# Performance work log

Hardware: AMD Instinct MI355X
Metric: run time of the kernel (lower is better)

The kernel has to match this reference:

```python
import jax, jax.numpy as jnp
import numpy as np

D_MODEL = 1024
HIDDEN = 1024
N_EXPERTS = 8
TOP_K = 2
BATCH, SEQ = 2, 2048
N_TOKENS = BATCH * SEQ


def setup_inputs() -> dict:
    key = jax.random.key(0)
    ks = jax.random.split(key, 6)
    x = jax.random.normal(ks[0], (BATCH, SEQ, D_MODEL), dtype=jnp.float32)
    expert_weights = jax.random.uniform(ks[1], (N_TOKENS, TOP_K), dtype=jnp.float32)
    expert_indices = jax.random.randint(ks[2], (N_TOKENS, TOP_K), 0, N_EXPERTS, dtype=jnp.int32)
    s_in = 1.0 / np.sqrt(D_MODEL)
    s_hid = 1.0 / np.sqrt(HIDDEN)
    w1 = jax.random.normal(ks[3], (N_EXPERTS, D_MODEL, HIDDEN), dtype=jnp.float32) * s_in
    w3 = jax.random.normal(ks[4], (N_EXPERTS, D_MODEL, HIDDEN), dtype=jnp.float32) * s_in
    w2 = jax.random.normal(ks[5], (N_EXPERTS, HIDDEN, D_MODEL), dtype=jnp.float32) * s_hid
    return {"x": x, "expert_weights": expert_weights, "expert_indices": expert_indices,
            "w1": w1, "w3": w3, "w2": w2}


def reference(x, expert_weights, expert_indices, w1, w3, w2):
    """Dropless MoE MLP (forward_once path): for each token t,
    out[t] = sum_k expert_weights[t,k] * SwiGLU_{expert_indices[t,k]}(x[t]).
    Also returns batch_size_per_expert (histogram of routed assignments).
    """
    d = x.shape[-1]
    xf = x.reshape(-1, d)                                  # [N, d]
    E = w1.shape[0]
    # combine[t, e] = sum over top-k slots routed to expert e of their weight
    onehot = jax.nn.one_hot(expert_indices, E, dtype=xf.dtype)       # [N, K, E]
    combine = jnp.einsum("nk,nke->ne", expert_weights, onehot)      # [N, E]
    out = jnp.zeros_like(xf)
    for e in range(E):  # fixed small loop over experts
        h = jax.nn.silu(xf @ w1[e]) * (xf @ w3[e])          # [N, H]
        out = out + combine[:, e:e + 1] * (h @ w2[e])       # [N, d]
    batch_size_per_expert = jnp.zeros((E,), dtype=jnp.int32).at[
        expert_indices.reshape(-1)].add(1)
    return out.reshape(x.shape), batch_size_per_expert
```

## Files before the change

### kernel.cpp

```cpp
#include <hip/hip_runtime.h>
#include <cstdint>

#define D 1024
#define N_TOKENS 4096
#define N_SLOTS 8192
#define NEXP 8
#define NKT 16
#define MAXT 80

typedef float f32x4 __attribute__((ext_vector_type(4)));
typedef __bf16 bf16x8 __attribute__((ext_vector_type(8)));
typedef __attribute__((address_space(3))) uint32_t lds_u32;
typedef __attribute__((address_space(1))) const uint32_t glb_u32;

__device__ __forceinline__ void gload_lds16(const void* g, void* l) {
  __builtin_amdgcn_global_load_lds((glb_u32*)g, (lds_u32*)l, 16, 0, 0);
}

__device__ __forceinline__ ushort f2bf(float f) {
  union { float f; uint32_t u; } c; c.f = f;
  uint32_t u = c.u;
  return (ushort)((u + 0x7FFFu + ((u >> 16) & 1u)) >> 16);
}

__device__ __forceinline__ float bf2f(ushort u) {
  union { uint32_t u; float f; } c; c.u = (uint32_t)u << 16;
  return c.f;
}

__device__ __forceinline__ bf16x8 lds_frag(const ushort* base, int row, int s) {
  return *(const bf16x8*)((const char*)base + row * 128 + ((s ^ (row & 7)) * 16));
}

#define TPAD 66

__global__ void prep_k(const float* __restrict__ x, const int* __restrict__ ei,
                       const float* __restrict__ ew,
                       const float* __restrict__ w1, const float* __restrict__ w3,
                       float* __restrict__ hist_out, int* __restrict__ meta,
                       int* __restrict__ tok, int* __restrict__ smap,
                       ushort* __restrict__ Xbf, ushort* __restrict__ w13t) {
  int bid = blockIdx.x, t = threadIdx.x;
  if (bid == 0) {
    __shared__ int cmat[256][8];
    __shared__ int off[NEXP + 1];
#pragma unroll
    for (int e = 0; e < NEXP; e++) cmat[t][e] = 0;
    int base = t * 32;
#pragma unroll 4
    for (int j = 0; j < 32; j++) cmat[t][ei[base + j]]++;
    __syncthreads();
    if (t < NEXP) {
      int run = 0;
      for (int i = 0; i < 256; i++) { int v = cmat[i][t]; cmat[i][t] = run; run += v; }
      meta[8 + t] = run;
    }
    __syncthreads();
    if (t == 0) {
      int s = 0;
      for (int e = 0; e < NEXP; e++) { off[e] = s; s += meta[8 + e]; }
      off[NEXP] = s;
      int nt = 0;
      for (int e = 0; e < NEXP; e++)
        for (int r = off[e]; r < off[e + 1]; r += 128)
          if (nt < MAXT) {
            meta[16 + nt] = e;
            meta[96 + nt] = r;
            int re = off[e + 1]; if (r + 128 < re) re = r + 128;
            meta[176 + nt] = re;
            nt++;
          }
      meta[0] = nt;
      for (int e = 0; e < NEXP; e++) hist_out[e] = (float)meta[8 + e];
    }
    __syncthreads();
#pragma unroll 4
    for (int j = 0; j < 32; j++) {
      int slot = base + j;
      int e = ei[slot];
      int p = off[e] + cmat[t][e]++;
      tok[p] = slot >> 1;
      smap[slot] = p;
    }
  } else if (bid <= 256) {
    int cb = bid - 1;
    const float4* xs = (const float4*)x + (size_t)cb * 4096;
    ushort4* xd = (ushort4*)Xbf + (size_t)cb * 4096;
#pragma unroll
    for (int i = 0; i < 16; i++) {
      float4 v = xs[i * 256 + t];
      ushort4 o;
      o.x = f2bf(v.x); o.y = f2bf(v.y); o.z = f2bf(v.z); o.w = f2bf(v.w);
      xd[i * 256 + t] = o;
    }
  } else {
    int wb = bid - 257;
    int z = wb >> 8, rem = wb & 255;
    int kb = rem >> 4, nb = rem & 15;
    int which = z >> 3, e = z & 7;
    const float* src = (which == 0 ? w1 : w3) + (size_t)e * D * D;
    ushort* dst = w13t + (size_t)e * 2048 * D;
    __shared__ ushort tile[64][TPAD];
    int k0 = kb * 64, n0 = nb * 64;
    int r = t >> 4, c = t & 15;
#pragma unroll
    for (int rep = 0; rep < 4; rep++) {
      int krow = rep * 16 + r;
      float4 v = *(const float4*)(src + (size_t)(k0 + krow) * D + n0 + c * 4);
      tile[krow][c * 4 + 0] = f2bf(v.x);
      tile[krow][c * 4 + 1] = f2bf(v.y);
      tile[krow][c * 4 + 2] = f2bf(v.z);
      tile[krow][c * 4 + 3] = f2bf(v.w);
    }
    __syncthreads();
#pragma unroll
    for (int rep = 0; rep < 4; rep++) {
      int lr = rep * 16 + r;
      int nrow = n0 + lr;
      ushort4 o;
      o.x = tile[c * 4 + 0][lr];
      o.y = tile[c * 4 + 1][lr];
      o.z = tile[c * 4 + 2][lr];
      o.w = tile[c * 4 + 3][lr];
      int crow = ((nrow >> 4) << 5) + ((which == 1) ? 16 : 0) + (nrow & 15);
      *(ushort4*)(dst + (size_t)crow * D + k0 + c * 4) = o;
    }
  }
}

__global__ __launch_bounds__(256, 4) void gemm1_k(
    const ushort* __restrict__ Xbf, const ushort* __restrict__ W13t,
    ushort* __restrict__ H, const int* __restrict__ tok,
    const int* __restrict__ meta,
    const float* __restrict__ w2, ushort* __restrict__ W2t) {
  __shared__ ushort sA[128 * 64];
  __shared__ ushort sB[128 * 64];
  int tm = blockIdx.y;
  int tid = threadIdx.x;

  if (tm >= MAXT) {
    int e = tm - MAXT;
    const float* src = w2 + (size_t)e * D * D;
    ushort* dst = W2t + (size_t)e * D * D;
    ushort (*tile)[TPAD] = (ushort(*)[TPAD])&sA[0];
    int kb = blockIdx.x;
    int r = tid >> 4, c = tid & 15;
    int k0 = kb * 64;
    for (int nb = 0; nb < 16; nb++) {
      int n0 = nb * 64;
      __syncthreads();
#pragma unroll
      for (int rep = 0; rep < 4; rep++) {
        int krow = rep * 16 + r;
        float4 v = *(const float4*)(src + (size_t)(k0 + krow) * D + n0 + c * 4);
        tile[krow][c * 4 + 0] = f2bf(v.x);
        tile[krow][c * 4 + 1] = f2bf(v.y);
        tile[krow][c * 4 + 2] = f2bf(v.z);
        tile[krow][c * 4 + 3] = f2bf(v.w);
      }
      __syncthreads();
#pragma unroll
      for (int rep = 0; rep < 4; rep++) {
        int lr = rep * 16 + r;
        ushort4 o;
        o.x = tile[c * 4 + 0][lr];
        o.y = tile[c * 4 + 1][lr];
        o.z = tile[c * 4 + 2][lr];
        o.w = tile[c * 4 + 3][lr];
        *(ushort4*)(dst + (size_t)(n0 + lr) * D + k0 + c * 4) = o;
      }
    }
    return;
  }
  if (tm >= meta[0]) return;

  int e = meta[16 + tm], r0 = meta[96 + tm], rend = meta[176 + tm];
  int n0i = blockIdx.x * 128;
  int lane = tid & 63, wid = tid >> 6;
  int wm = wid >> 1, wn = wid & 1;

  const char* gX = (const char*)Xbf;
  const char* gB = (const char*)(W13t + (size_t)e * 2048 * D);

  int prow = tid >> 3, pslot = tid & 7;
  size_t arow[4];
  int brow[4], phys[4];
#pragma unroll
  for (int i = 0; i < 4; i++) {
    int row = i * 32 + prow;
    int gr = r0 + row; if (gr > N_SLOTS - 1) gr = N_SLOTS - 1;
    arow[i] = (size_t)tok[gr] * 2048;
    brow[i] = n0i + row;
    phys[i] = (pslot ^ (row & 7)) * 16;
  }

  f32x4 acc[4][4] = {};

  for (int kt = 0; kt < NKT; kt++) {
    int kb = kt * 128;
#pragma unroll
    for (int i = 0; i < 4; i++) {
      gload_lds16(gX + arow[i] + kb + phys[i], (char*)sA + (i * 256 + tid) * 16);
      gload_lds16(gB + (size_t)brow[i] * 2048 + kb + phys[i],
                  (char*)sB + (i * 256 + tid) * 16);
    }
    __syncthreads();
#pragma unroll
    for (int kk = 0; kk < 2; kk++) {
      int s = kk * 4 + (lane >> 4);
      bf16x8 a[4], b[4];
#pragma unroll
      for (int mf = 0; mf < 4; mf++)
        a[mf] = lds_frag(sA, wm * 64 + mf * 16 + (lane & 15), s);
#pragma unroll
      for (int nf = 0; nf < 4; nf++)
        b[nf] = lds_frag(sB, wn * 64 + nf * 16 + (lane & 15), s);
#pragma unroll
      for (int mf = 0; mf < 4; mf++)
#pragma unroll
        for (int nf = 0; nf < 4; nf++)
          acc[mf][nf] = __builtin_amdgcn_mfma_f32_16x16x32_bf16(a[mf], b[nf], acc[mf][nf], 0, 0, 0);
    }
    __syncthreads();
  }

  int cb = (n0i >> 1) + wn * 32 + (lane & 15);
#pragma unroll
  for (int mf = 0; mf < 4; mf++)
#pragma unroll
    for (int v = 0; v < 4; v++) {
      int r = r0 + wm * 64 + mf * 16 + (lane >> 4) * 4 + v;
      if (r >= rend) continue;
#pragma unroll
      for (int p = 0; p < 2; p++) {
        float g = acc[mf][2 * p][v], u = acc[mf][2 * p + 1][v];
        float hv = g / (1.f + __expf(-g)) * u;
        H[(size_t)r * D + cb + p * 16] = f2bf(hv);
      }
    }
}

__global__ __launch_bounds__(256, 4) void gemm2_k(
    const ushort* __restrict__ Hm, const ushort* __restrict__ W2t,
    ushort* __restrict__ Y, const int* __restrict__ meta) {
  __shared__ ushort sA[128 * 64];
  __shared__ ushort sB[128 * 64];
  int tm = blockIdx.y;
  if (tm >= meta[0]) return;
  int e = meta[16 + tm], r0 = meta[96 + tm], rend = meta[176 + tm];
  int n0 = blockIdx.x * 128;
  int tid = threadIdx.x, lane = tid & 63, wid = tid >> 6;
  int wm = wid >> 1, wn = wid & 1;

  const char* gH = (const char*)Hm;
  const char* gB = (const char*)(W2t + (size_t)e * D * D);

  int prow = tid >> 3, pslot = tid & 7;
  size_t arow[4];
  int brow[4], phys[4];
#pragma unroll
  for (int i = 0; i < 4; i++) {
    int row = i * 32 + prow;
    int gr = r0 + row; if (gr > N_SLOTS - 1) gr = N_SLOTS - 1;
    arow[i] = (size_t)gr * 2048;
    brow[i] = n0 + row;
    phys[i] = (pslot ^ (row & 7)) * 16;
  }

  f32x4 acc[4][4] = {};

  for (int kt = 0; kt < NKT; kt++) {
    int kb = kt * 128;
#pragma unroll
    for (int i = 0; i < 4; i++) {
      gload_lds16(gH + arow[i] + kb + phys[i], (char*)sA + (i * 256 + tid) * 16);
      gload_lds16(gB + (size_t)brow[i] * 2048 + kb + phys[i],
                  (char*)sB + (i * 256 + tid) * 16);
    }
    __syncthreads();
#pragma unroll
    for (int kk = 0; kk < 2; kk++) {
      int s = kk * 4 + (lane >> 4);
      bf16x8 a[4], b[4];
#pragma unroll
      for (int mf = 0; mf < 4; mf++)
        a[mf] = lds_frag(sA, wm * 64 + mf * 16 + (lane & 15), s);
#pragma unroll
      for (int nf = 0; nf < 4; nf++)
        b[nf] = lds_frag(sB, wn * 64 + nf * 16 + (lane & 15), s);
#pragma unroll
      for (int mf = 0; mf < 4; mf++)
#pragma unroll
        for (int nf = 0; nf < 4; nf++)
          acc[mf][nf] = __builtin_amdgcn_mfma_f32_16x16x32_bf16(a[mf], b[nf], acc[mf][nf], 0, 0, 0);
    }
    __syncthreads();
  }

#pragma unroll
  for (int mf = 0; mf < 4; mf++)
#pragma unroll
    for (int v = 0; v < 4; v++) {
      int r = r0 + wm * 64 + mf * 16 + (lane >> 4) * 4 + v;
      if (r >= rend) continue;
#pragma unroll
      for (int nf = 0; nf < 4; nf++)
        Y[(size_t)r * D + n0 + wn * 64 + nf * 16 + (lane & 15)] = f2bf(acc[mf][nf][v]);
    }
}

__global__ void combine_k(const ushort* __restrict__ Y, const int* __restrict__ smap,
                          const float* __restrict__ ew, float* __restrict__ out) {
  int tkn = blockIdx.x * 4 + (threadIdx.x >> 6);
  int lane = threadIdx.x & 63;
  int p0 = smap[2 * tkn], p1 = smap[2 * tkn + 1];
  float w0 = ew[2 * tkn], w1 = ew[2 * tkn + 1];
  const ushort4* y0 = (const ushort4*)(Y + (size_t)p0 * D);
  const ushort4* y1 = (const ushort4*)(Y + (size_t)p1 * D);
  float4* o = (float4*)(out + (size_t)tkn * D);
#pragma unroll
  for (int j = 0; j < 4; j++) {
    int c = j * 64 + lane;
    ushort4 a = y0[c], b = y1[c];
    float4 v;
    v.x = w0 * bf2f(a.x) + w1 * bf2f(b.x);
    v.y = w0 * bf2f(a.y) + w1 * bf2f(b.y);
    v.z = w0 * bf2f(a.z) + w1 * bf2f(b.z);
    v.w = w0 * bf2f(a.w) + w1 * bf2f(b.w);
    o[c] = v;
  }
}

extern "C" void kernel_launch(void* const* d_in, const int* in_sizes, int n_in,
                              void* d_out, int out_size, void* d_ws, size_t ws_size,
                              hipStream_t stream) {
  const float* x  = (const float*)d_in[0];
  const float* ew = (const float*)d_in[1];
  const int*   ei = (const int*)d_in[2];
  const float* w1 = (const float*)d_in[3];
  const float* w3 = (const float*)d_in[4];
  const float* w2 = (const float*)d_in[5];
  float* out = (float*)d_out;

  char* ws = (char*)d_ws;
  int*    meta = (int*)ws;
  int*    tok  = (int*)(ws + 4096);
  int*    smap = (int*)(ws + 4096 + 32768);
  ushort* Xbf  = (ushort*)(ws + (1ull << 20));
  ushort* W13t = (ushort*)(ws + (9ull << 20));
  ushort* W2t  = (ushort*)(ws + (41ull << 20));
  ushort* Hm   = (ushort*)(ws + (57ull << 20));
  ushort* Ym   = (ushort*)(ws + (1ull << 20));

  prep_k<<<4353, 256, 0, stream>>>(x, ei, ew, w1, w3,
                                   out + (size_t)N_TOKENS * D, meta, tok, smap,
                                   Xbf, W13t);
  gemm1_k<<<dim3(16, MAXT + 8), 256, 0, stream>>>(Xbf, W13t, Hm, tok, meta, w2, W2t);
  gemm2_k<<<dim3(8, MAXT), 256, 0, stream>>>(Hm, W2t, Ym, meta);
  combine_k<<<N_TOKENS / 4, 256, 0, stream>>>(Ym, smap, ew, out);
}
```

Before: 116.0 us.

## Fuse combine into gemm2 via weighted atomicAdd and spread W2 transpose blocks

```diff
diff --git a/kernel.cpp b/kernel.cpp
--- a/kernel.cpp
+++ b/kernel.cpp
@@ -7,6 +7,7 @@
 #define NEXP 8
 #define NKT 16
 #define MAXT 80
+#define NTRF 128
 
 typedef float f32x4 __attribute__((ext_vector_type(4)));
 typedef __bf16 bf16x8 __attribute__((ext_vector_type(8)));
@@ -38,8 +39,9 @@
                        const float* __restrict__ ew,
                        const float* __restrict__ w1, const float* __restrict__ w3,
                        float* __restrict__ hist_out, int* __restrict__ meta,
-                       int* __restrict__ tok, int* __restrict__ smap,
-                       ushort* __restrict__ Xbf, ushort* __restrict__ w13t) {
+                       int* __restrict__ tok, float* __restrict__ wgt,
+                       ushort* __restrict__ Xbf, ushort* __restrict__ w13t,
+                       float* __restrict__ out) {
   int bid = blockIdx.x, t = threadIdx.x;
   if (bid == 0) {
     __shared__ int cmat[256][8];
@@ -80,18 +82,21 @@
       int e = ei[slot];
       int p = off[e] + cmat[t][e]++;
       tok[p] = slot >> 1;
-      smap[slot] = p;
+      wgt[p] = ew[slot];
     }
   } else if (bid <= 256) {
     int cb = bid - 1;
     const float4* xs = (const float4*)x + (size_t)cb * 4096;
     ushort4* xd = (ushort4*)Xbf + (size_t)cb * 4096;
+    float4* oz = (float4*)out + (size_t)cb * 4096;
+    float4 z; z.x = 0.f; z.y = 0.f; z.z = 0.f; z.w = 0.f;
 #pragma unroll
     for (int i = 0; i < 16; i++) {
       float4 v = xs[i * 256 + t];
       ushort4 o;
       o.x = f2bf(v.x); o.y = f2bf(v.y); o.z = f2bf(v.z); o.w = f2bf(v.w);
       xd[i * 256 + t] = o;
+      oz[i * 256 + t] = z;
     }
   } else {
     int wb = bid - 257;
@@ -138,40 +143,38 @@
   int tm = blockIdx.y;
   int tid = threadIdx.x;
 
-  if (tm >= MAXT) {
-    int e = tm - MAXT;
+  if (tm < NTRF) {
+    int T = tm * 16 + blockIdx.x;
+    int e = T >> 8, rem = T & 255;
+    int kb = rem >> 4, nb = rem & 15;
     const float* src = w2 + (size_t)e * D * D;
     ushort* dst = W2t + (size_t)e * D * D;
     ushort (*tile)[TPAD] = (ushort(*)[TPAD])&sA[0];
-    int kb = blockIdx.x;
     int r = tid >> 4, c = tid & 15;
-    int k0 = kb * 64;
-    for (int nb = 0; nb < 16; nb++) {
-      int n0 = nb * 64;
-      __syncthreads();
-#pragma unroll
-      for (int rep = 0; rep < 4; rep++) {
-        int krow = rep * 16 + r;
-        float4 v = *(const float4*)(src + (size_t)(k0 + krow) * D + n0 + c * 4);
-        tile[krow][c * 4 + 0] = f2bf(v.x);
-        tile[krow][c * 4 + 1] = f2bf(v.y);
-        tile[krow][c * 4 + 2] = f2bf(v.z);
-        tile[krow][c * 4 + 3] = f2bf(v.w);
-      }
-      __syncthreads();
-#pragma unroll
-      for (int rep = 0; rep < 4; rep++) {
-        int lr = rep * 16 + r;
-        ushort4 o;
-        o.x = tile[c * 4 + 0][lr];
-        o.y = tile[c * 4 + 1][lr];
-        o.z = tile[c * 4 + 2][lr];
-        o.w = tile[c * 4 + 3][lr];
-        *(ushort4*)(dst + (size_t)(n0 + lr) * D + k0 + c * 4) = o;
-      }
+    int k0 = kb * 64, n0 = nb * 64;
+#pragma unroll
+    for (int rep = 0; rep < 4; rep++) {
+      int krow = rep * 16 + r;
+      float4 v = *(const float4*)(src + (size_t)(k0 + krow) * D + n0 + c * 4);
+      tile[krow][c * 4 + 0] = f2bf(v.x);
+      tile[krow][c * 4 + 1] = f2bf(v.y);
+      tile[krow][c * 4 + 2] = f2bf(v.z);
+      tile[krow][c * 4 + 3] = f2bf(v.w);
+    }
+    __syncthreads();
+#pragma unroll
+    for (int rep = 0; rep < 4; rep++) {
+      int lr = rep * 16 + r;
+      ushort4 o;
+      o.x = tile[c * 4 + 0][lr];
+      o.y = tile[c * 4 + 1][lr];
+      o.z = tile[c * 4 + 2][lr];
+      o.w = tile[c * 4 + 3][lr];
+      *(ushort4*)(dst + (size_t)(n0 + lr) * D + k0 + c * 4) = o;
     }
     return;
   }
+  tm -= NTRF;
   if (tm >= meta[0]) return;
 
   int e = meta[16 + tm], r0 = meta[96 + tm], rend = meta[176 + tm];
@@ -242,7 +245,8 @@
 
 __global__ __launch_bounds__(256, 4) void gemm2_k(
     const ushort* __restrict__ Hm, const ushort* __restrict__ W2t,
-    ushort* __restrict__ Y, const int* __restrict__ meta) {
+    const int* __restrict__ tok, const float* __restrict__ wgt,
+    float* __restrict__ out, const int* __restrict__ meta) {
   __shared__ ushort sA[128 * 64];
   __shared__ ushort sB[128 * 64];
   int tm = blockIdx.y;
@@ -303,32 +307,13 @@
     for (int v = 0; v < 4; v++) {
       int r = r0 + wm * 64 + mf * 16 + (lane >> 4) * 4 + v;
       if (r >= rend) continue;
+      int tokid = tok[r];
+      float w = wgt[r];
+      float* orow = out + (size_t)tokid * D + n0 + wn * 64 + (lane & 15);
 #pragma unroll
       for (int nf = 0; nf < 4; nf++)
-        Y[(size_t)r * D + n0 + wn * 64 + nf * 16 + (lane & 15)] = f2bf(acc[mf][nf][v]);
-    }
-}
-
-__global__ void combine_k(const ushort* __restrict__ Y, const int* __restrict__ smap,
-                          const float* __restrict__ ew, float* __restrict__ out) {
-  int tkn = blockIdx.x * 4 + (threadIdx.x >> 6);
-  int lane = threadIdx.x & 63;
-  int p0 = smap[2 * tkn], p1 = smap[2 * tkn + 1];
-  float w0 = ew[2 * tkn], w1 = ew[2 * tkn + 1];
-  const ushort4* y0 = (const ushort4*)(Y + (size_t)p0 * D);
-  const ushort4* y1 = (const ushort4*)(Y + (size_t)p1 * D);
-  float4* o = (float4*)(out + (size_t)tkn * D);
-#pragma unroll
-  for (int j = 0; j < 4; j++) {
-    int c = j * 64 + lane;
-    ushort4 a = y0[c], b = y1[c];
-    float4 v;
-    v.x = w0 * bf2f(a.x) + w1 * bf2f(b.x);
-    v.y = w0 * bf2f(a.y) + w1 * bf2f(b.y);
-    v.z = w0 * bf2f(a.z) + w1 * bf2f(b.z);
-    v.w = w0 * bf2f(a.w) + w1 * bf2f(b.w);
-    o[c] = v;
-  }
+        atomicAdd(orow + nf * 16, w * acc[mf][nf][v]);
+    }
 }
 
 extern "C" void kernel_launch(void* const* d_in, const int* in_sizes, int n_in,
@@ -345,17 +330,15 @@
   char* ws = (char*)d_ws;
   int*    meta = (int*)ws;
   int*    tok  = (int*)(ws + 4096);
-  int*    smap = (int*)(ws + 4096 + 32768);
+  float*  wgt  = (float*)(ws + 4096 + 32768);
   ushort* Xbf  = (ushort*)(ws + (1ull << 20));
   ushort* W13t = (ushort*)(ws + (9ull << 20));
   ushort* W2t  = (ushort*)(ws + (41ull << 20));
   ushort* Hm   = (ushort*)(ws + (57ull << 20));
-  ushort* Ym   = (ushort*)(ws + (1ull << 20));
 
   prep_k<<<4353, 256, 0, stream>>>(x, ei, ew, w1, w3,
-                                   out + (size_t)N_TOKENS * D, meta, tok, smap,
-                                   Xbf, W13t);
-  gemm1_k<<<dim3(16, MAXT + 8), 256, 0, stream>>>(Xbf, W13t, Hm, tok, meta, w2, W2t);
-  gemm2_k<<<dim3(8, MAXT), 256, 0, stream>>>(Hm, W2t, Ym, meta);
-  combine_k<<<N_TOKENS / 4, 256, 0, stream>>>(Ym, smap, ew, out);
-}
+                                   out + (size_t)N_TOKENS * D, meta, tok, wgt,
+                                   Xbf, W13t, out);
+  gemm1_k<<<dim3(16, NTRF + MAXT), 256, 0, stream>>>(Xbf, W13t, Hm, tok, meta, w2, W2t);
+  gemm2_k<<<dim3(8, MAXT), 256, 0, stream>>>(Hm, W2t, tok, wgt, out, meta);
+}
```

New measurement: 137.5 us. +18.5%, slower.

## Schedule W2 transpose blocks first and prefetch next tile in registers

Applied to the files above, without the earlier changes.

```diff
diff --git a/kernel.cpp b/kernel.cpp
--- a/kernel.cpp
+++ b/kernel.cpp
@@ -7,6 +7,7 @@
 #define NEXP 8
 #define NKT 16
 #define MAXT 80
+#define NTRF 8
 
 typedef float f32x4 __attribute__((ext_vector_type(4)));
 typedef __bf16 bf16x8 __attribute__((ext_vector_type(8)));
@@ -138,40 +139,78 @@
   int tm = blockIdx.y;
   int tid = threadIdx.x;
 
-  if (tm >= MAXT) {
-    int e = tm - MAXT;
+  if (tm < NTRF) {
+    int gid = tm * 16 + blockIdx.x;
+    int e = gid >> 4, kb = gid & 15;
     const float* src = w2 + (size_t)e * D * D;
     ushort* dst = W2t + (size_t)e * D * D;
     ushort (*tile)[TPAD] = (ushort(*)[TPAD])&sA[0];
-    int kb = blockIdx.x;
     int r = tid >> 4, c = tid & 15;
     int k0 = kb * 64;
-    for (int nb = 0; nb < 16; nb++) {
-      int n0 = nb * 64;
+    const float* sp = src + (size_t)k0 * D + c * 4;
+    float4 va[4], vb[4];
+#pragma unroll
+    for (int rep = 0; rep < 4; rep++)
+      va[rep] = *(const float4*)(sp + (size_t)(rep * 16 + r) * D);
+    for (int i = 0; i < 16; i += 2) {
       __syncthreads();
 #pragma unroll
       for (int rep = 0; rep < 4; rep++) {
         int krow = rep * 16 + r;
-        float4 v = *(const float4*)(src + (size_t)(k0 + krow) * D + n0 + c * 4);
-        tile[krow][c * 4 + 0] = f2bf(v.x);
-        tile[krow][c * 4 + 1] = f2bf(v.y);
-        tile[krow][c * 4 + 2] = f2bf(v.z);
-        tile[krow][c * 4 + 3] = f2bf(v.w);
+        tile[krow][c * 4 + 0] = f2bf(va[rep].x);
+        tile[krow][c * 4 + 1] = f2bf(va[rep].y);
+        tile[krow][c * 4 + 2] = f2bf(va[rep].z);
+        tile[krow][c * 4 + 3] = f2bf(va[rep].w);
+      }
+      if (i + 1 < 16)
+#pragma unroll
+        for (int rep = 0; rep < 4; rep++)
+          vb[rep] = *(const float4*)(sp + (size_t)(rep * 16 + r) * D + (i + 1) * 64);
+      __syncthreads();
+      {
+        int n0 = i * 64;
+#pragma unroll
+        for (int rep = 0; rep < 4; rep++) {
+          int lr = rep * 16 + r;
+          ushort4 o;
+          o.x = tile[c * 4 + 0][lr];
+          o.y = tile[c * 4 + 1][lr];
+          o.z = tile[c * 4 + 2][lr];
+          o.w = tile[c * 4 + 3][lr];
+          *(ushort4*)(dst + (size_t)(n0 + lr) * D + k0 + c * 4) = o;
+        }
       }
       __syncthreads();
 #pragma unroll
       for (int rep = 0; rep < 4; rep++) {
-        int lr = rep * 16 + r;
-        ushort4 o;
-        o.x = tile[c * 4 + 0][lr];
-        o.y = tile[c * 4 + 1][lr];
-        o.z = tile[c * 4 + 2][lr];
-        o.w = tile[c * 4 + 3][lr];
-        *(ushort4*)(dst + (size_t)(n0 + lr) * D + k0 + c * 4) = o;
+        int krow = rep * 16 + r;
+        tile[krow][c * 4 + 0] = f2bf(vb[rep].x);
+        tile[krow][c * 4 + 1] = f2bf(vb[rep].y);
+        tile[krow][c * 4 + 2] = f2bf(vb[rep].z);
+        tile[krow][c * 4 + 3] = f2bf(vb[rep].w);
       }
+      if (i + 2 < 16)
+#pragma unroll
+        for (int rep = 0; rep < 4; rep++)
+          va[rep] = *(const float4*)(sp + (size_t)(rep * 16 + r) * D + (i + 2) * 64);
+      __syncthreads();
+      {
+        int n0 = (i + 1) * 64;
+#pragma unroll
+        for (int rep = 0; rep < 4; rep++) {
+          int lr = rep * 16 + r;
+          ushort4 o;
+          o.x = tile[c * 4 + 0][lr];
+          o.y = tile[c * 4 + 1][lr];
+          o.z = tile[c * 4 + 2][lr];
+          o.w = tile[c * 4 + 3][lr];
+          *(ushort4*)(dst + (size_t)(n0 + lr) * D + k0 + c * 4) = o;
+        }
+      }
     }
     return;
   }
+  tm -= NTRF;
   if (tm >= meta[0]) return;
 
   int e = meta[16 + tm], r0 = meta[96 + tm], rend = meta[176 + tm];
@@ -355,7 +394,7 @@
   prep_k<<<4353, 256, 0, stream>>>(x, ei, ew, w1, w3,
                                    out + (size_t)N_TOKENS * D, meta, tok, smap,
                                    Xbf, W13t);
-  gemm1_k<<<dim3(16, MAXT + 8), 256, 0, stream>>>(Xbf, W13t, Hm, tok, meta, w2, W2t);
+  gemm1_k<<<dim3(16, NTRF + MAXT), 256, 0, stream>>>(Xbf, W13t, Hm, tok, meta, w2, W2t);
   gemm2_k<<<dim3(8, MAXT), 256, 0, stream>>>(Hm, W2t, Ym, meta);
   combine_k<<<N_TOKENS / 4, 256, 0, stream>>>(Ym, smap, ew, out);
 }
```

New measurement: 115.5 us. No clear change (-0.5%).
